# Performance work log

Measured on AMD Instinct MI355X. Metric: run time of the kernel, lower is better.

The kernel has to match this reference:

```python
import jax, jax.numpy as jnp
import numpy as np

B, S, E, H, DH, F = 4, 2048, 1024, 4, 256, 4096


def setup_inputs() -> dict:
    key = jax.random.key(0)
    ks = jax.random.split(key, 16)
    def w(k, shape):
        return jax.random.normal(k, shape, jnp.float32) * 0.02
    return {
        "inputs": jax.random.normal(ks[0], (B, S, E), jnp.float32),
        "context": jax.random.normal(ks[1], (B, S, E), jnp.float32),
        # self-attention (causal) per-head projections stacked over heads
        "Wk1": w(ks[2], (H, E, DH)), "bk1": jnp.zeros((H, DH), jnp.float32),
        "Wq1": w(ks[3], (H, E, DH)), "bq1": jnp.zeros((H, DH), jnp.float32),
        "Wv1": w(ks[4], (H, E, DH)), "bv1": jnp.zeros((H, DH), jnp.float32),
        "Wo1": w(ks[5], (E, E)), "bo1": jnp.zeros((E,), jnp.float32),
        # cross-attention (no mask)
        "Wk2": w(ks[6], (H, E, DH)), "bk2": jnp.zeros((H, DH), jnp.float32),
        "Wq2": w(ks[7], (H, E, DH)), "bq2": jnp.zeros((H, DH), jnp.float32),
        "Wv2": w(ks[8], (H, E, DH)), "bv2": jnp.zeros((H, DH), jnp.float32),
        "Wo2": w(ks[9], (E, E)), "bo2": jnp.zeros((E,), jnp.float32),
        "ln_g": jnp.ones((E,), jnp.float32), "ln_b": jnp.zeros((E,), jnp.float32),
        # FFN
        "W1": w(ks[10], (E, F)), "b1": jnp.zeros((F,), jnp.float32),
        "W2": w(ks[11], (F, E)), "b2": jnp.zeros((E,), jnp.float32),
    }


def _mha(kin, vin, qin, Wk, bk, Wq, bq, Wv, bv, Wo, bo, causal):
    # per-head Dense projections, batched over heads: [B,S,E] x [H,E,DH] -> [B,H,S,DH]
    K = jnp.einsum('bse,hed->bhsd', kin, Wk) + bk[None, :, None, :]
    Q = jnp.einsum('bse,hed->bhsd', qin, Wq) + bq[None, :, None, :]
    V = jnp.einsum('bse,hed->bhsd', vin, Wv) + bv[None, :, None, :]
    # NOTE: original divides by head_dim (K.get_shape()[2]), NOT sqrt(head_dim)
    scores = jnp.einsum('bhqd,bhkd->bhqk', Q, K) / K.shape[-1]
    if causal:
        sq, sk = scores.shape[-2], scores.shape[-1]
        mask = jnp.triu(jnp.full((sq, sk), -jnp.inf, scores.dtype), k=1)
        scores = scores + mask  # additive -inf strictly above the diagonal
    A = jax.nn.softmax(scores, axis=-1)
    # concat heads in order along the feature axis, then output Dense
    out = jnp.einsum('bhqk,bhkd->bqhd', A, V).reshape(qin.shape[0], qin.shape[1], -1)
    return out @ Wo + bo


def _ln(x, g, b):
    # keras LayerNormalization default epsilon = 1e-3
    m = x.mean(-1, keepdims=True)
    v = ((x - m) ** 2).mean(-1, keepdims=True)
    return (x - m) / jnp.sqrt(v + 1e-3) * g + b


def reference(inputs, context, Wk1, bk1, Wq1, bq1, Wv1, bv1, Wo1, bo1,
              Wk2, bk2, Wq2, bq2, Wv2, bv2, Wo2, bo2,
              ln_g, ln_b, W1, b1, W2, b2):
    # dropout layers are identity at inference
    a = _mha(inputs, inputs, inputs, Wk1, bk1, Wq1, bq1, Wv1, bv1, Wo1, bo1, True) + inputs
    a = _ln(a, ln_g, ln_b)
    # cross-attention: keys/values = context, queries = normalized self-attn output
    c = _mha(context, context, a, Wk2, bk2, Wq2, bq2, Wv2, bv2, Wo2, bo2, False) + a
    c = _ln(c, ln_g, ln_b)
    h = jax.nn.relu(c @ W1 + b1) @ W2 + b2 + c
    return jax.nn.relu(_ln(h, ln_g, ln_b))
```

## Files before the change

### kernel.cpp

```cpp
#include <hip/hip_runtime.h>

#define DEV __device__ __forceinline__

typedef unsigned short u16;
typedef __bf16 bf16x8 __attribute__((ext_vector_type(8)));
typedef bf16x8 __attribute__((may_alias)) bf16x8a;
typedef float f32x4 __attribute__((ext_vector_type(4)));
typedef float f32x16 __attribute__((ext_vector_type(16)));

constexpr int NB = 4, NS = 2048, NE = 1024, NH = 4, NDH = 256, NF = 4096;
constexpr int NR = NB * NS;

DEV u16 f2bf(float f) {
  unsigned u = __float_as_uint(f);
  u += 0x7fff + ((u >> 16) & 1);
  return (u16)(u >> 16);
}

DEV f32x4 mfma16(bf16x8 a, bf16x8 b, f32x4 c) {
  return __builtin_amdgcn_mfma_f32_16x16x32_bf16(a, b, c, 0, 0, 0);
}
DEV f32x16 mfma32(bf16x8 a, bf16x8 b, f32x16 c) {
  return __builtin_amdgcn_mfma_f32_32x32x16_bf16(a, b, c, 0, 0, 0);
}

DEV bf16x8 ldfrag(const u16* p) { return *(const bf16x8a*)p; }

DEV void gload_lds16(const void* g, void* l) {
  __builtin_amdgcn_global_load_lds(
      (const __attribute__((address_space(1))) void*)g,
      (__attribute__((address_space(3))) void*)l, 16, 0, 0);
}

DEV void blockbar() {
  asm volatile("" ::: "memory");
  __builtin_amdgcn_s_barrier();
  asm volatile("" ::: "memory");
}

DEV unsigned packbf(float a, float b) {
  union { __bf16 h[2]; unsigned u; } x;
  x.h[0] = (__bf16)a; x.h[1] = (__bf16)b;
  return x.u;
}

__global__ void cast_f32_bf16(const float* __restrict__ in, u16* __restrict__ out, int n4) {
  int i = blockIdx.x * 256 + threadIdx.x;
  if (i >= n4) return;
  float4 v = ((const float4*)in)[i];
  ushort4 o;
  o.x = f2bf(v.x); o.y = f2bf(v.y); o.z = f2bf(v.z); o.w = f2bf(v.w);
  ((ushort4*)out)[i] = o;
}

__global__ void transpose_cast(const float* __restrict__ in, u16* __restrict__ out, int R, int C) {
  __shared__ float t[32][33];
  size_t base = (size_t)blockIdx.z * R * C;
  int c0 = blockIdx.x * 32, r0 = blockIdx.y * 32;
  int x = threadIdx.x;
  for (int yy = threadIdx.y; yy < 32; yy += 8)
    t[yy][x] = in[base + (size_t)(r0 + yy) * C + c0 + x];
  __syncthreads();
  for (int yy = threadIdx.y; yy < 32; yy += 8)
    out[base + (size_t)(c0 + yy) * R + r0 + x] = f2bf(t[x][yy]);
}

__global__ void transpose_v(const u16* __restrict__ V, int vstride, u16* __restrict__ Vt) {
  __shared__ u16 t[32][34];
  int bh = blockIdx.z, b = bh >> 2, h = bh & (NH - 1);
  int s0 = blockIdx.x * 32, d0 = blockIdx.y * 32;
  int x = threadIdx.x;
  for (int yy = threadIdx.y; yy < 32; yy += 8)
    t[yy][x] = V[(size_t)(b * NS + s0 + yy) * vstride + h * NDH + d0 + x];
  __syncthreads();
  for (int yy = threadIdx.y; yy < 32; yy += 8)
    Vt[((size_t)bh * NDH + d0 + yy) * NS + s0 + x] = t[x][yy];
}

__global__ void copy_f32(const float* __restrict__ s, float* __restrict__ d, int n) {
  int i = blockIdx.x * 256 + threadIdx.x;
  if (i < n) d[i] = s[i];
}

template<int OUTF32, int RELU>
__global__ __launch_bounds__(256, 2)
void gemm2b(const u16* __restrict__ A, const u16* __restrict__ Bt,
            const float* __restrict__ bias, const float* __restrict__ res,
            float* __restrict__ outF, u16* __restrict__ outB,
            int M, int N, int K)
{
  __shared__ __align__(16) u16 smem[32768];

  int tid = threadIdx.x, w = tid >> 6, lane = tid & 63;
  int lr = lane & 15, lk = lane >> 4;

  int flat = blockIdx.y * gridDim.x + blockIdx.x;
  int cpx = (gridDim.x * gridDim.y) >> 3;
  int swz = (flat & 7) * cpx + (flat >> 3);
  int bx = swz % gridDim.x, by = swz / gridDim.x;
  int rowBlk = by * 128, colBlk = bx * 128;

  f32x4 acc[8][2];
#pragma unroll
  for (int f = 0; f < 8; f++)
#pragma unroll
    for (int n = 0; n < 2; n++) acc[f][n] = (f32x4){0.f, 0.f, 0.f, 0.f};

  int srow = lane >> 3;
  int scol = ((lane & 7) ^ srow) * 8;

  const u16* gA = A + (size_t)rowBlk * K;
  const u16* gB = Bt + (size_t)colBlk * K;

  auto stageA = [&](int t, int p) {
#pragma unroll
    for (int j = 0; j < 4; j++) {
      int rbase = (w * 4 + j) * 8;
      gload_lds16(gA + (size_t)(rbase + srow) * K + (size_t)t * 64 + scol,
                  &smem[(p * 128 + rbase) * 64]);
    }
  };
  auto stageB = [&](int t, int p) {
#pragma unroll
    for (int j = 0; j < 4; j++) {
      int rbase = (w * 4 + j) * 8;
      gload_lds16(gB + (size_t)(rbase + srow) * K + (size_t)t * 64 + scol,
                  &smem[16384 + (p * 128 + rbase) * 64]);
    }
  };

  stageB(0, 0);
  asm volatile("" ::: "memory");
  stageA(0, 0);
  asm volatile("s_waitcnt vmcnt(0)" ::: "memory");
  blockbar();

  int NT = K >> 6;
  for (int t = 0; t < NT; t++) {
    int p = t & 1;
    if (t + 1 < NT) {
      stageB(t + 1, p ^ 1);
      asm volatile("" ::: "memory");
      stageA(t + 1, p ^ 1);
      asm volatile("" ::: "memory");
    }
    const u16* Ar = &smem[p * 8192];
    const u16* Br = &smem[16384 + p * 8192];
    bf16x8 bf[2][2], af[8][2];
#pragma unroll
    for (int n = 0; n < 2; n++)
#pragma unroll
      for (int s = 0; s < 2; s++) {
        int rowB = w * 32 + n * 16 + lr;
        bf[n][s] = ldfrag(&Br[rowB * 64 + (((s * 4 + lk) ^ (lr & 7)) * 8)]);
      }
#pragma unroll
    for (int f = 0; f < 8; f++)
#pragma unroll
      for (int s = 0; s < 2; s++) {
        int rowA = f * 16 + lr;
        af[f][s] = ldfrag(&Ar[rowA * 64 + (((s * 4 + lk) ^ (lr & 7)) * 8)]);
      }
    __builtin_amdgcn_s_setprio(1);
#pragma unroll
    for (int f = 0; f < 8; f++)
#pragma unroll
      for (int n = 0; n < 2; n++)
#pragma unroll
        for (int s = 0; s < 2; s++)
          acc[f][n] = mfma16(af[f][s], bf[n][s], acc[f][n]);
    __builtin_amdgcn_s_setprio(0);
    asm volatile("s_waitcnt vmcnt(0)" ::: "memory");
    blockbar();
  }

  int ocol0 = colBlk + w * 32;
#pragma unroll
  for (int n = 0; n < 2; n++) {
    int c = ocol0 + n * 16 + lr;
    float bv = bias[c];
#pragma unroll
    for (int f = 0; f < 8; f++) {
      int r0 = rowBlk + f * 16 + lk * 4;
#pragma unroll
      for (int j = 0; j < 4; j++) {
        float v = acc[f][n][j] + bv;
        if (OUTF32) v += res[(size_t)(r0 + j) * N + c];
        if (RELU) v = fmaxf(v, 0.f);
        if (OUTF32) outF[(size_t)(r0 + j) * N + c] = v;
        else        outB[(size_t)(r0 + j) * N + c] = f2bf(v);
      }
    }
  }
}

template<int CAUSAL, int SPLIT>
__global__ __launch_bounds__(512, 2)
void attn8w(const u16* __restrict__ Qp, int qstride,
            const u16* __restrict__ Kp, int kstride,
            const u16* __restrict__ Vt, u16* __restrict__ O,
            float* __restrict__ Op, float* __restrict__ ml)
{
  __shared__ __align__(16) u16 smem[65536];

  int bidx = blockIdx.x;
  int bh, qt, kt0, kt1;
  if (SPLIT) {
    int qtIdx = bidx >> 5;
    qt = 15 - qtIdx;
    int sub = bidx & 31;
    int half = sub >> 4;
    bh = sub & 15;
    kt0 = half ? (qt + 1) : 0;
    kt1 = half ? (2 * qt + 2) : (qt + 1);
  } else {
    bh = bidx & 15;
    qt = CAUSAL ? (15 - (bidx >> 4)) : (bidx >> 4);
    kt0 = 0;
    kt1 = CAUSAL ? (2 * qt + 2) : (NS / 64);
  }
  int b = bh >> 2, h = bh & 3;
  int tid = threadIdx.x, w = tid >> 6, lane = tid & 63;
  int L = lane & 31, hi = lane >> 5;
  int g = w >> 1, ks = w & 1;

  int qbase = qt * 128 + g * 32;

  const u16* qrow = Qp + (size_t)(b * NS + qbase + L) * qstride + h * NDH;
  bf16x8 qf[16];
#pragma unroll
  for (int s = 0; s < 16; s++) qf[s] = ldfrag(qrow + s * 16 + hi * 8);

  f32x16 oacc[8];
#pragma unroll
  for (int db = 0; db < 8; db++) oacc[db] = (f32x16){};
  float m = -1e30f, l = 0.f;

  constexpr float SC = 1.0f / NDH;

  const u16* kbase = Kp + (size_t)(b * NS) * kstride + h * NDH;
  const u16* vbase = Vt + (size_t)bh * NDH * NS;

  auto stage = [&](int kt, int buf) {
#pragma unroll
    for (int ii = 0; ii < 4; ii++) {
      int gi = w * 4 + ii;
      int krow = 2 * gi + hi;
      int kcol = L ^ (krow & 31);
      gload_lds16(kbase + (size_t)(kt * 64 + krow) * kstride + kcol * 8,
                  &smem[buf * 16384 + gi * 512]);
      int vd = gi * 8 + (lane >> 3);
      int vg = (lane & 7) ^ (vd & 7);
      gload_lds16(vbase + (size_t)vd * NS + kt * 64 + vg * 8,
                  &smem[32768 + buf * 16384 + gi * 512]);
    }
  };

  stage(kt0, 0);
  asm volatile("" ::: "memory");

  for (int kt = kt0; kt < kt1; kt++) {
    int buf = (kt - kt0) & 1;
    const u16* bK = &smem[buf * 16384];
    const u16* bV = &smem[32768 + buf * 16384];
    if (kt + 1 < kt1) {
      stage(kt + 1, buf ^ 1);
      asm volatile("s_waitcnt vmcnt(8)" ::: "memory");
    } else {
      asm volatile("s_waitcnt vmcnt(0)" ::: "memory");
    }
    blockbar();

    int ksub0 = kt * 64 + ks * 32;
    bool skip = CAUSAL && (ksub0 > qbase + 31);
    if (!skip) {
      bool domask = CAUSAL && (ksub0 + 31 > qbase);
      __builtin_amdgcn_s_setprio(1);
      f32x16 sa = (f32x16){};
#pragma unroll
      for (int s = 0; s < 16; s++) {
        int row = ks * 32 + L;
        bf16x8 kf = ldfrag(&bK[row * 256 + (((2 * s + hi) ^ L) & 31) * 8]);
        sa = mfma32(kf, qf[s], sa);
      }
      __builtin_amdgcn_s_setprio(0);

      float p[16];
      float tmax = -1e30f;
#pragma unroll
      for (int r = 0; r < 16; r++) {
        float v = sa[r] * SC;
        if (domask) {
          int key = ksub0 + (r & 3) + 8 * (r >> 2) + 4 * hi;
          if (key > qbase + L) v = -1e30f;
        }
        p[r] = v;
        tmax = fmaxf(tmax, v);
      }
      tmax = fmaxf(tmax, __shfl_xor(tmax, 32));

      float mn = m;
      if (!__all(tmax - m <= 5.0f)) {
        mn = fmaxf(m, tmax);
        float rs = __expf(m - mn);
        m = mn;
        l *= rs;
#pragma unroll
        for (int db = 0; db < 8; db++)
#pragma unroll
          for (int r = 0; r < 16; r++) oacc[db][r] *= rs;
      }
      float psum = 0.f;
#pragma unroll
      for (int r = 0; r < 16; r++) {
        p[r] = __expf(p[r] - mn);
        psum += p[r];
      }
      psum += __shfl_xor(psum, 32);
      l += psum;

      unsigned pk01 = packbf(p[0], p[1]),  pk23 = packbf(p[2], p[3]);
      unsigned pk45 = packbf(p[4], p[5]),  pk67 = packbf(p[6], p[7]);
      unsigned pk89 = packbf(p[8], p[9]),  pkab = packbf(p[10], p[11]);
      unsigned pkcd = packbf(p[12], p[13]), pkef = packbf(p[14], p[15]);
      unsigned s45 = (unsigned)__shfl_xor((int)pk45, 32);
      unsigned s67 = (unsigned)__shfl_xor((int)pk67, 32);
      unsigned s01 = (unsigned)__shfl_xor((int)pk01, 32);
      unsigned s23 = (unsigned)__shfl_xor((int)pk23, 32);
      unsigned scd = (unsigned)__shfl_xor((int)pkcd, 32);
      unsigned sef = (unsigned)__shfl_xor((int)pkef, 32);
      unsigned s89 = (unsigned)__shfl_xor((int)pk89, 32);
      unsigned sab = (unsigned)__shfl_xor((int)pkab, 32);
      union { unsigned u[4]; bf16x8 v; } fb0, fb1;
      fb0.u[0] = hi ? s45 : pk01;
      fb0.u[1] = hi ? s67 : pk23;
      fb0.u[2] = hi ? pk45 : s01;
      fb0.u[3] = hi ? pk67 : s23;
      fb1.u[0] = hi ? scd : pk89;
      fb1.u[1] = hi ? sef : pkab;
      fb1.u[2] = hi ? pkcd : s89;
      fb1.u[3] = hi ? pkef : sab;
      bf16x8 pb0 = fb0.v, pb1 = fb1.v;

      __builtin_amdgcn_s_setprio(1);
#pragma unroll
      for (int db = 0; db < 8; db++) {
        int vd = db * 32 + L;
        bf16x8 vf0 = ldfrag(&bV[vd * 64 + (((ks * 4 + hi) ^ (vd & 7)) & 7) * 8]);
        bf16x8 vf1 = ldfrag(&bV[vd * 64 + (((ks * 4 + 2 + hi) ^ (vd & 7)) & 7) * 8]);
        oacc[db] = mfma32(vf0, pb0, oacc[db]);
        oacc[db] = mfma32(vf1, pb1, oacc[db]);
      }
      __builtin_amdgcn_s_setprio(0);
    }
    blockbar();
  }

  float* fsm = (float*)smem;
  blockbar();
  if (hi == 0) { fsm[w * 64 + L * 2] = m; fsm[w * 64 + L * 2 + 1] = l; }
  asm volatile("s_waitcnt lgkmcnt(0)" ::: "memory");
  blockbar();
  float mb = fsm[(w ^ 1) * 64 + L * 2];
  float lb = fsm[(w ^ 1) * 64 + L * 2 + 1];
  float M = fmaxf(m, mb);
  float eo = __expf(m - M);
  float lt = l * eo + lb * __expf(mb - M);
  asm volatile("s_waitcnt lgkmcnt(0)" ::: "memory");
  blockbar();
  float* reg = fsm + g * 8192;
  if (w & 1) {
#pragma unroll
    for (int db = 0; db < 8; db++)
#pragma unroll
      for (int r = 0; r < 16; r++) {
        int d = db * 32 + (r & 3) + 8 * (r >> 2) + 4 * hi;
        reg[d * 32 + L] = oacc[db][r] * eo;
      }
  }
  asm volatile("s_waitcnt lgkmcnt(0)" ::: "memory");
  blockbar();
  if (!(w & 1)) {
    if (SPLIT) {
      float* OpB = Op + (size_t)bidx * 32768 + (size_t)(g * 32 + L) * 256;
      if (hi == 0) {
        ml[((size_t)bidx * 128 + g * 32 + L) * 2]     = M;
        ml[((size_t)bidx * 128 + g * 32 + L) * 2 + 1] = lt;
      }
#pragma unroll
      for (int db = 0; db < 8; db++) {
#pragma unroll
        for (int rq = 0; rq < 4; rq++) {
          int d0 = db * 32 + rq * 8 + hi * 4;
          float4 v;
          v.x = oacc[db][rq * 4 + 0] * eo + reg[(d0 + 0) * 32 + L];
          v.y = oacc[db][rq * 4 + 1] * eo + reg[(d0 + 1) * 32 + L];
          v.z = oacc[db][rq * 4 + 2] * eo + reg[(d0 + 2) * 32 + L];
          v.w = oacc[db][rq * 4 + 3] * eo + reg[(d0 + 3) * 32 + L];
          *(float4*)(OpB + d0) = v;
        }
      }
    } else {
      float inv = 1.f / lt;
      size_t orow = (size_t)(b * NS + qbase + L) * NE + h * NDH;
#pragma unroll
      for (int db = 0; db < 8; db++) {
#pragma unroll
        for (int rq = 0; rq < 4; rq++) {
          int d0 = db * 32 + rq * 8 + hi * 4;
          float a0 = (oacc[db][rq * 4 + 0] * eo + reg[(d0 + 0) * 32 + L]) * inv;
          float a1 = (oacc[db][rq * 4 + 1] * eo + reg[(d0 + 1) * 32 + L]) * inv;
          float a2 = (oacc[db][rq * 4 + 2] * eo + reg[(d0 + 2) * 32 + L]) * inv;
          float a3 = (oacc[db][rq * 4 + 3] * eo + reg[(d0 + 3) * 32 + L]) * inv;
          uint2 wv;
          wv.x = packbf(a0, a1);
          wv.y = packbf(a2, a3);
          *(uint2*)&O[orow + d0] = wv;
        }
      }
    }
  }
}

__global__ __launch_bounds__(256)
void merge_attn(const float* __restrict__ Op, const float* __restrict__ ml,
                u16* __restrict__ O)
{
  int blk = blockIdx.x;
  int qt = blk >> 4, bh = blk & 15;
  int b = bh >> 2, h = bh & 3;
  int p0 = (15 - qt) * 32 + bh;
  int p1 = p0 + 16;
  int tid = threadIdx.x;
  int row = tid >> 1;
  int dbase = (tid & 1) * 128;

  float m0 = ml[((size_t)p0 * 128 + row) * 2];
  float l0 = ml[((size_t)p0 * 128 + row) * 2 + 1];
  float m1 = ml[((size_t)p1 * 128 + row) * 2];
  float l1 = ml[((size_t)p1 * 128 + row) * 2 + 1];
  float M = fmaxf(m0, m1);
  float e0 = __expf(m0 - M), e1 = __expf(m1 - M);
  float inv = 1.f / (l0 * e0 + l1 * e1);
  const float* O0 = Op + ((size_t)p0 * 128 + row) * 256 + dbase;
  const float* O1 = Op + ((size_t)p1 * 128 + row) * 256 + dbase;
  u16* dst = O + (size_t)(b * NS + qt * 128 + row) * NE + h * NDH + dbase;
#pragma unroll
  for (int d = 0; d < 128; d += 4) {
    float4 a = *(const float4*)(O0 + d);
    float4 c = *(const float4*)(O1 + d);
    uint2 wv;
    wv.x = packbf((a.x * e0 + c.x * e1) * inv, (a.y * e0 + c.y * e1) * inv);
    wv.y = packbf((a.z * e0 + c.z * e1) * inv, (a.w * e0 + c.w * e1) * inv);
    *(uint2*)(dst + d) = wv;
  }
}

template<int RELU, int WBF>
__global__ __launch_bounds__(256)
void ln_kernel(const float* __restrict__ x, const float* __restrict__ g,
               const float* __restrict__ bb, float* __restrict__ outF,
               u16* __restrict__ outB)
{
  int row = blockIdx.x, tid = threadIdx.x;
  float4 v = ((const float4*)(x + (size_t)row * NE))[tid];
  float s = v.x + v.y + v.z + v.w;
  float s2 = v.x * v.x + v.y * v.y + v.z * v.z + v.w * v.w;
#pragma unroll
  for (int off = 32; off; off >>= 1) {
    s += __shfl_xor(s, off);
    s2 += __shfl_xor(s2, off);
  }
  __shared__ float red[8];
  int wid = tid >> 6, lane = tid & 63;
  if (lane == 0) { red[wid] = s; red[4 + wid] = s2; }
  __syncthreads();
  s = red[0] + red[1] + red[2] + red[3];
  s2 = red[4] + red[5] + red[6] + red[7];
  float mean = s * (1.f / NE);
  float var = s2 * (1.f / NE) - mean * mean;
  float rstd = rsqrtf(var + 1e-3f);
  float4 gg = ((const float4*)g)[tid];
  float4 bv = ((const float4*)bb)[tid];
  float4 o;
  o.x = (v.x - mean) * rstd * gg.x + bv.x;
  o.y = (v.y - mean) * rstd * gg.y + bv.y;
  o.z = (v.z - mean) * rstd * gg.z + bv.z;
  o.w = (v.w - mean) * rstd * gg.w + bv.w;
  if (RELU) {
    o.x = fmaxf(o.x, 0.f); o.y = fmaxf(o.y, 0.f);
    o.z = fmaxf(o.z, 0.f); o.w = fmaxf(o.w, 0.f);
  }
  ((float4*)(outF + (size_t)row * NE))[tid] = o;
  if (WBF) {
    ushort4 ob;
    ob.x = f2bf(o.x); ob.y = f2bf(o.y); ob.z = f2bf(o.z); ob.w = f2bf(o.w);
    ((ushort4*)(outB + (size_t)row * NE))[tid] = ob;
  }
}

constexpr size_t OFF_X    = 0;
constexpr size_t OFF_W    = OFF_X + 16777216;
constexpr size_t OFF_BIAS = OFF_W + 33554432;
constexpr size_t OFF_QKV  = OFF_BIAS + 32768;
constexpr size_t OFF_VT   = OFF_QKV + 50331648;
constexpr size_t OFF_T0   = OFF_VT + 16777216;
constexpr size_t OFF_A    = OFF_T0 + 33554432;
constexpr size_t OFF_ABF  = OFF_A + 33554432;

extern "C" void kernel_launch(void* const* d_in, const int* in_sizes, int n_in,
                              void* d_out, int out_size, void* d_ws, size_t ws_size,
                              hipStream_t stream) {
  (void)in_sizes; (void)n_in; (void)out_size; (void)ws_size;
  const float* inp = (const float*)d_in[0];
  const float* ctx = (const float*)d_in[1];
  const float* Wk1 = (const float*)d_in[2];  const float* bk1 = (const float*)d_in[3];
  const float* Wq1 = (const float*)d_in[4];  const float* bq1 = (const float*)d_in[5];
  const float* Wv1 = (const float*)d_in[6];  const float* bv1 = (const float*)d_in[7];
  const float* Wo1 = (const float*)d_in[8];  const float* bo1 = (const float*)d_in[9];
  const float* Wk2 = (const float*)d_in[10]; const float* bk2 = (const float*)d_in[11];
  const float* Wq2 = (const float*)d_in[12]; const float* bq2 = (const float*)d_in[13];
  const float* Wv2 = (const float*)d_in[14]; const float* bv2 = (const float*)d_in[15];
  const float* Wo2 = (const float*)d_in[16]; const float* bo2 = (const float*)d_in[17];
  const float* lng = (const float*)d_in[18]; const float* lnb = (const float*)d_in[19];
  const float* W1  = (const float*)d_in[20]; const float* b1  = (const float*)d_in[21];
  const float* W2  = (const float*)d_in[22]; const float* b2  = (const float*)d_in[23];
  float* out = (float*)d_out;
  char* ws = (char*)d_ws;

  u16* XBF    = (u16*)(ws + OFF_X);
  u16* WQKV1T = (u16*)(ws + OFF_W);
  u16* WKV2T  = WQKV1T + 3072 * 1024;
  u16* WQ2T   = WKV2T + 2048 * 1024;
  u16* WO1T   = WQ2T + 1024 * 1024;
  u16* WO2T   = WO1T + 1024 * 1024;
  u16* W1T    = WO2T + 1024 * 1024;
  u16* W2T    = W1T + 4096 * 1024;
  float* BQKV1 = (float*)(ws + OFF_BIAS);
  float* BKV2  = BQKV1 + 3072;
  u16* QKV  = (u16*)(ws + OFF_QKV);
  u16* Q2   = QKV + 8192 * 2048;
  u16* VT   = (u16*)(ws + OFF_VT);
  u16* MID  = QKV;
  float* T0 = (float*)(ws + OFF_T0);
  float* OpBuf = T0;
  float* Af = (float*)(ws + OFF_A);
  u16* ABF  = (u16*)(ws + OFF_ABF);
  float* MlBuf = (float*)(ws + OFF_ABF);
  u16* Obuf = XBF;

  dim3 tb(32, 8);

  cast_f32_bf16<<<8192, 256, 0, stream>>>(inp, XBF, NR * NE / 4);
  transpose_cast<<<dim3(8, 32, 4), tb, 0, stream>>>(Wk1, WQKV1T,               NE, NDH);
  transpose_cast<<<dim3(8, 32, 4), tb, 0, stream>>>(Wq1, WQKV1T + 1024 * 1024, NE, NDH);
  transpose_cast<<<dim3(8, 32, 4), tb, 0, stream>>>(Wv1, WQKV1T + 2048 * 1024, NE, NDH);
  transpose_cast<<<dim3(32, 32, 1), tb, 0, stream>>>(Wo1, WO1T, NE, NE);
  transpose_cast<<<dim3(8, 32, 4), tb, 0, stream>>>(Wk2, WKV2T,               NE, NDH);
  transpose_cast<<<dim3(8, 32, 4), tb, 0, stream>>>(Wv2, WKV2T + 1024 * 1024, NE, NDH);
  transpose_cast<<<dim3(8, 32, 4), tb, 0, stream>>>(Wq2, WQ2T, NE, NDH);
  transpose_cast<<<dim3(32, 32, 1), tb, 0, stream>>>(Wo2, WO2T, NE, NE);
  transpose_cast<<<dim3(128, 32, 1), tb, 0, stream>>>(W1, W1T, NE, NF);
  transpose_cast<<<dim3(32, 128, 1), tb, 0, stream>>>(W2, W2T, NF, NE);
  copy_f32<<<4, 256, 0, stream>>>(bk1, BQKV1, 1024);
  copy_f32<<<4, 256, 0, stream>>>(bq1, BQKV1 + 1024, 1024);
  copy_f32<<<4, 256, 0, stream>>>(bv1, BQKV1 + 2048, 1024);
  copy_f32<<<4, 256, 0, stream>>>(bk2, BKV2, 1024);
  copy_f32<<<4, 256, 0, stream>>>(bv2, BKV2 + 1024, 1024);

  gemm2b<0, 0><<<dim3(24, 64), 256, 0, stream>>>(XBF, WQKV1T, BQKV1, nullptr,
                                                 nullptr, QKV, NR, 3072, NE);
  transpose_v<<<dim3(64, 8, 16), tb, 0, stream>>>(QKV + 2048, 3072, VT);
  attn8w<1, 1><<<512, 512, 0, stream>>>(QKV + 1024, 3072, QKV, 3072, VT,
                                        nullptr, OpBuf, MlBuf);
  merge_attn<<<256, 256, 0, stream>>>(OpBuf, MlBuf, Obuf);
  gemm2b<1, 0><<<dim3(8, 64), 256, 0, stream>>>(Obuf, WO1T, bo1, inp,
                                                T0, nullptr, NR, NE, NE);
  ln_kernel<0, 1><<<NR, 256, 0, stream>>>(T0, lng, lnb, Af, ABF);

  cast_f32_bf16<<<8192, 256, 0, stream>>>(ctx, XBF, NR * NE / 4);
  gemm2b<0, 0><<<dim3(16, 64), 256, 0, stream>>>(XBF, WKV2T, BKV2, nullptr,
                                                 nullptr, QKV, NR, 2048, NE);
  gemm2b<0, 0><<<dim3(8, 64), 256, 0, stream>>>(ABF, WQ2T, bq2, nullptr,
                                                nullptr, Q2, NR, NE, NE);
  transpose_v<<<dim3(64, 8, 16), tb, 0, stream>>>(QKV + 1024, 2048, VT);
  attn8w<0, 0><<<256, 512, 0, stream>>>(Q2, 1024, QKV, 2048, VT, Obuf,
                                        nullptr, nullptr);
  gemm2b<1, 0><<<dim3(8, 64), 256, 0, stream>>>(Obuf, WO2T, bo2, Af,
                                                T0, nullptr, NR, NE, NE);
  ln_kernel<0, 1><<<NR, 256, 0, stream>>>(T0, lng, lnb, Af, ABF);

  gemm2b<0, 1><<<dim3(32, 64), 256, 0, stream>>>(ABF, W1T, b1, nullptr,
                                                 nullptr, MID, NR, NF, NE);
  gemm2b<1, 0><<<dim3(8, 64), 256, 0, stream>>>(MID, W2T, b2, Af,
                                                T0, nullptr, NR, NE, NF);
  ln_kernel<1, 0><<<NR, 256, 0, stream>>>(T0, lng, lnb, out, nullptr);
}
```

Before: 713.0 us.

## Pipeline GEMM with 4-slot half-K ring buffer and partial vmcnt waits

Replaces the 2-stage double buffer (K=64 per stage) in the bf16 GEMM with a 4-slot ring of K=32 slices, prefetching two slices ahead. The wait uses partial vmcnt counts, so the loads for later slices stay in flight while the current slice is consumed, and only one barrier is needed per iteration. This is meant to hide global-load latency better than the previous full vmcnt(0) wait. The trade-off is twice as many barriers per K and less MFMA work between them. The LDS swizzle changes to a 4-way XOR to fit the narrower rows.

After: 744.3 us. 4.4% more time.

```diff
diff --git a/kernel.cpp b/kernel.cpp
--- a/kernel.cpp
+++ b/kernel.cpp
@@ -84,10 +84,10 @@
 
 template<int OUTF32, int RELU>
 __global__ __launch_bounds__(256, 2)
-void gemm2b(const u16* __restrict__ A, const u16* __restrict__ Bt,
-            const float* __restrict__ bias, const float* __restrict__ res,
-            float* __restrict__ outF, u16* __restrict__ outB,
-            int M, int N, int K)
+void gemm_c2(const u16* __restrict__ A, const u16* __restrict__ Bt,
+             const float* __restrict__ bias, const float* __restrict__ res,
+             float* __restrict__ outF, u16* __restrict__ outB,
+             int M, int N, int K)
 {
   __shared__ __align__(16) u16 smem[32768];
 
@@ -106,72 +106,82 @@
 #pragma unroll
     for (int n = 0; n < 2; n++) acc[f][n] = (f32x4){0.f, 0.f, 0.f, 0.f};
 
-  int srow = lane >> 3;
-  int scol = ((lane & 7) ^ srow) * 8;
-
   const u16* gA = A + (size_t)rowBlk * K;
   const u16* gB = Bt + (size_t)colBlk * K;
 
-  auto stageA = [&](int t, int p) {
-#pragma unroll
-    for (int j = 0; j < 4; j++) {
-      int rbase = (w * 4 + j) * 8;
-      gload_lds16(gA + (size_t)(rbase + srow) * K + (size_t)t * 64 + scol,
-                  &smem[(p * 128 + rbase) * 64]);
+  int srow = lane >> 2;
+  int sgl = lane & 3;
+
+  auto stageA = [&](int hs) {
+    int reg = hs & 3;
+    int k0 = hs * 32;
+#pragma unroll
+    for (int j = 0; j < 2; j++) {
+      int rbase = (w * 2 + j) * 16;
+      int row = rbase + srow;
+      int gl = sgl ^ (row & 3);
+      gload_lds16(gA + (size_t)row * K + k0 + gl * 8,
+                  &smem[reg * 4096 + rbase * 32]);
     }
   };
-  auto stageB = [&](int t, int p) {
-#pragma unroll
-    for (int j = 0; j < 4; j++) {
-      int rbase = (w * 4 + j) * 8;
-      gload_lds16(gB + (size_t)(rbase + srow) * K + (size_t)t * 64 + scol,
-                  &smem[16384 + (p * 128 + rbase) * 64]);
+  auto stageB = [&](int hs) {
+    int reg = hs & 3;
+    int k0 = hs * 32;
+#pragma unroll
+    for (int j = 0; j < 2; j++) {
+      int rbase = (w * 2 + j) * 16;
+      int row = rbase + srow;
+      int gl = sgl ^ (row & 3);
+      gload_lds16(gB + (size_t)row * K + k0 + gl * 8,
+                  &smem[16384 + reg * 4096 + rbase * 32]);
     }
   };
 
-  stageB(0, 0);
+  stageA(0);
   asm volatile("" ::: "memory");
-  stageA(0, 0);
-  asm volatile("s_waitcnt vmcnt(0)" ::: "memory");
-  blockbar();
-
-  int NT = K >> 6;
-  for (int t = 0; t < NT; t++) {
-    int p = t & 1;
-    if (t + 1 < NT) {
-      stageB(t + 1, p ^ 1);
+  stageB(0);
+  asm volatile("" ::: "memory");
+  stageA(1);
+  asm volatile("" ::: "memory");
+  stageB(1);
+  asm volatile("" ::: "memory");
+
+  int NHs = K >> 5;
+  for (int hs = 0; hs < NHs; hs++) {
+    if (hs + 2 < NHs) {
+      stageA(hs + 2);
       asm volatile("" ::: "memory");
-      stageA(t + 1, p ^ 1);
+      stageB(hs + 2);
       asm volatile("" ::: "memory");
     }
-    const u16* Ar = &smem[p * 8192];
-    const u16* Br = &smem[16384 + p * 8192];
-    bf16x8 bf[2][2], af[8][2];
-#pragma unroll
-    for (int n = 0; n < 2; n++)
-#pragma unroll
-      for (int s = 0; s < 2; s++) {
-        int rowB = w * 32 + n * 16 + lr;
-        bf[n][s] = ldfrag(&Br[rowB * 64 + (((s * 4 + lk) ^ (lr & 7)) * 8)]);
-      }
+    int rem = NHs - 1 - hs;
+    if (rem > 2) rem = 2;
+    if (rem == 2)      asm volatile("s_waitcnt vmcnt(8)" ::: "memory");
+    else if (rem == 1) asm volatile("s_waitcnt vmcnt(4)" ::: "memory");
+    else               asm volatile("s_waitcnt vmcnt(0)" ::: "memory");
+    blockbar();
+
+    int reg = hs & 3;
+    const u16* Ar = &smem[reg * 4096];
+    const u16* Br = &smem[16384 + reg * 4096];
+    bf16x8 bf[2], af[8];
+#pragma unroll
+    for (int n = 0; n < 2; n++) {
+      int rowB = w * 32 + n * 16 + lr;
+      bf[n] = ldfrag(&Br[rowB * 32 + ((lk ^ (lr & 3)) * 8)]);
+    }
+#pragma unroll
+    for (int f = 0; f < 8; f++) {
+      int rowA = f * 16 + lr;
+      af[f] = ldfrag(&Ar[rowA * 32 + ((lk ^ (lr & 3)) * 8)]);
+    }
+    __builtin_amdgcn_s_setprio(1);
 #pragma unroll
     for (int f = 0; f < 8; f++)
 #pragma unroll
-      for (int s = 0; s < 2; s++) {
-        int rowA = f * 16 + lr;
-        af[f][s] = ldfrag(&Ar[rowA * 64 + (((s * 4 + lk) ^ (lr & 7)) * 8)]);
-      }
-    __builtin_amdgcn_s_setprio(1);
-#pragma unroll
-    for (int f = 0; f < 8; f++)
-#pragma unroll
       for (int n = 0; n < 2; n++)
-#pragma unroll
-        for (int s = 0; s < 2; s++)
-          acc[f][n] = mfma16(af[f][s], bf[n][s], acc[f][n]);
+        acc[f][n] = mfma16(af[f], bf[n], acc[f][n]);
     __builtin_amdgcn_s_setprio(0);
-    asm volatile("s_waitcnt vmcnt(0)" ::: "memory");
-    blockbar();
   }
 
   int ocol0 = colBlk + w * 32;
@@ -568,31 +578,31 @@
   copy_f32<<<4, 256, 0, stream>>>(bk2, BKV2, 1024);
   copy_f32<<<4, 256, 0, stream>>>(bv2, BKV2 + 1024, 1024);
 
-  gemm2b<0, 0><<<dim3(24, 64), 256, 0, stream>>>(XBF, WQKV1T, BQKV1, nullptr,
-                                                 nullptr, QKV, NR, 3072, NE);
+  gemm_c2<0, 0><<<dim3(24, 64), 256, 0, stream>>>(XBF, WQKV1T, BQKV1, nullptr,
+                                                  nullptr, QKV, NR, 3072, NE);
   transpose_v<<<dim3(64, 8, 16), tb, 0, stream>>>(QKV + 2048, 3072, VT);
   attn8w<1, 1><<<512, 512, 0, stream>>>(QKV + 1024, 3072, QKV, 3072, VT,
                                         nullptr, OpBuf, MlBuf);
   merge_attn<<<256, 256, 0, stream>>>(OpBuf, MlBuf, Obuf);
-  gemm2b<1, 0><<<dim3(8, 64), 256, 0, stream>>>(Obuf, WO1T, bo1, inp,
-                                                T0, nullptr, NR, NE, NE);
+  gemm_c2<1, 0><<<dim3(8, 64), 256, 0, stream>>>(Obuf, WO1T, bo1, inp,
+                                                 T0, nullptr, NR, NE, NE);
   ln_kernel<0, 1><<<NR, 256, 0, stream>>>(T0, lng, lnb, Af, ABF);
 
   cast_f32_bf16<<<8192, 256, 0, stream>>>(ctx, XBF, NR * NE / 4);
-  gemm2b<0, 0><<<dim3(16, 64), 256, 0, stream>>>(XBF, WKV2T, BKV2, nullptr,
-                                                 nullptr, QKV, NR, 2048, NE);
-  gemm2b<0, 0><<<dim3(8, 64), 256, 0, stream>>>(ABF, WQ2T, bq2, nullptr,
-                                                nullptr, Q2, NR, NE, NE);
+  gemm_c2<0, 0><<<dim3(16, 64), 256, 0, stream>>>(XBF, WKV2T, BKV2, nullptr,
+                                                  nullptr, QKV, NR, 2048, NE);
+  gemm_c2<0, 0><<<dim3(8, 64), 256, 0, stream>>>(ABF, WQ2T, bq2, nullptr,
+                                                 nullptr, Q2, NR, NE, NE);
   transpose_v<<<dim3(64, 8, 16), tb, 0, stream>>>(QKV + 1024, 2048, VT);
   attn8w<0, 0><<<256, 512, 0, stream>>>(Q2, 1024, QKV, 2048, VT, Obuf,
                                         nullptr, nullptr);
-  gemm2b<1, 0><<<dim3(8, 64), 256, 0, stream>>>(Obuf, WO2T, bo2, Af,
-                                                T0, nullptr, NR, NE, NE);
+  gemm_c2<1, 0><<<dim3(8, 64), 256, 0, stream>>>(Obuf, WO2T, bo2, Af,
+                                                 T0, nullptr, NR, NE, NE);
   ln_kernel<0, 1><<<NR, 256, 0, stream>>>(T0, lng, lnb, Af, ABF);
 
-  gemm2b<0, 1><<<dim3(32, 64), 256, 0, stream>>>(ABF, W1T, b1, nullptr,
-                                                 nullptr, MID, NR, NF, NE);
-  gemm2b<1, 0><<<dim3(8, 64), 256, 0, stream>>>(MID, W2T, b2, Af,
-                                                T0, nullptr, NR, NE, NF);
+  gemm_c2<0, 1><<<dim3(32, 64), 256, 0, stream>>>(ABF, W1T, b1, nullptr,
+                                                  nullptr, MID, NR, NF, NE);
+  gemm_c2<1, 0><<<dim3(8, 64), 256, 0, stream>>>(MID, W2T, b2, Af,
+                                                 T0, nullptr, NR, NE, NF);
   ln_kernel<1, 0><<<NR, 256, 0, stream>>>(T0, lng, lnb, out, nullptr);
 }
```
